# Kernel optimization log

Hardware: AMD Instinct MI355X
Metric: run time of the kernel (lower is better)

Reference implementation:

```python
import jax, jax.numpy as jnp
import numpy as np

N_ATOMS = 20000
N_CG = 1000
N_EDGES = 200000
FEAT = 128
N_RBF = 20
N_CONV = 3
CUTOFF = 5.0
EPS = 1e-15


def swish(x):
    return x * jax.nn.sigmoid(x)


def preprocess_r(r):
    # r: (n, 3) -> dist (n,), unit (n, 3)
    d = jnp.sqrt((r * r + EPS).sum(-1))
    return d, r / d[:, None]


def dist_embed(d, W, b):
    # PainnRadialBasis (learnable_k=False) + Dense + cosine envelope
    k = jnp.arange(1, N_RBF + 1, dtype=d.dtype)
    rbf = jnp.sin(k[None, :] * jnp.pi * d[:, None] / CUTOFF) / d[:, None]
    env = 0.5 * (jnp.cos(jnp.pi * d / CUTOFF) + 1.0) * (d < CUTOFF).astype(d.dtype)
    return (rbf @ W + b) * env[:, None]


def scatter_mean(x, idx, n):
    s = jax.ops.segment_sum(x, idx, num_segments=n)
    cnt = jax.ops.segment_sum(jnp.ones(idx.shape[0], x.dtype), idx, num_segments=n)
    cnt = jnp.maximum(cnt, 1.0)
    return s / cnt.reshape((n,) + (1,) * (x.ndim - 1))


def cg_encoder(z, xyz, cg_xyz, mapping, nbr_list, embed,
               msg_W1, msg_b1, msg_W2, msg_b2, msg_distW, msg_distb,
               upd_U, upd_V, upd_W1, upd_b1, upd_W2, upd_b2,
               cg_W1, cg_b1, cg_W2, cg_b2, cg_distW, cg_distb):
    s = embed[z]                                     # (N, F)
    v = jnp.zeros((s.shape[0], FEAT, 3), s.dtype)    # (N, F, 3)
    src, dst = nbr_list[:, 0], nbr_list[:, 1]
    r_ij = xyz[dst] - xyz[src]
    r_iI = xyz - cg_xyz[mapping]
    d_ij, u_ij = preprocess_r(r_ij)
    d_iI, u_iI = preprocess_r(r_iI)

    S_I = None
    V_I = None
    for i in range(N_CONV):
        # ---- MessageBlock ----
        phi = swish(s @ msg_W1[i] + msg_b1[i]) @ msg_W2[i] + msg_b2[i]          # (N, 3F)
        w_s = dist_embed(d_ij, msg_distW[i], msg_distb[i])                      # (E, 3F)
        inv = (phi[dst] * w_s).reshape(-1, 3, FEAT)                             # (E, 3, F)
        dv_ij = inv[:, 2, :, None] * u_ij[:, None, :] + inv[:, 0, :, None] * v[dst]
        s = s + jax.ops.segment_sum(inv[:, 1, :], src, num_segments=N_ATOMS)
        v = v + jax.ops.segment_sum(dv_ij, src, num_segments=N_ATOMS)
        # ---- UpdateBlock ----
        u_v = jnp.einsum('nfd,fg->ngd', v, upd_U[i])
        v_v = jnp.einsum('nfd,fg->ngd', v, upd_V[i])
        v_v_norm = jnp.sqrt((v_v * v_v + EPS).sum(-1))                          # (N, F)
        stack = swish(jnp.concatenate([s, v_v_norm], -1) @ upd_W1[i] + upd_b1[i]) @ upd_W2[i] + upd_b2[i]
        a_vv = stack[:, :FEAT, None]
        a_sv = stack[:, FEAT:2 * FEAT]
        a_ss = stack[:, 2 * FEAT:]
        v = v + u_v * a_vv
        s = s + (u_v * v_v).sum(-1) * a_sv + a_ss
        # ---- init CG features after first conv ----
        if i == 0:
            S_I = scatter_mean(s, mapping, N_CG)
            V_I = jnp.zeros((N_CG, FEAT, 3), s.dtype)
        # ---- ContractiveMessageBlock ----
        phi_cg = swish(s @ cg_W1[i] + cg_b1[i]) @ cg_W2[i] + cg_b2[i]           # (N, 3F)
        w_cg = dist_embed(d_iI, cg_distW[i], cg_distb[i])
        inv_cg = (phi_cg * w_cg).reshape(-1, 3, FEAT)
        dv_iI = inv_cg[:, 2, :, None] * u_iI[:, None, :] + inv_cg[:, 0, :, None] * v
        S_I = S_I + scatter_mean(inv_cg[:, 1, :], mapping, N_CG)
        V_I = V_I + scatter_mean(dv_iI, mapping, N_CG)
    return S_I


def setup_inputs() -> dict:
    key = jax.random.key(0)
    ks = jax.random.split(key, 20)
    p = lambda i, shape: jax.random.normal(ks[i], shape, jnp.float32) * 0.05
    return {
        'z': jax.random.randint(ks[0], (N_ATOMS,), 1, 100),
        'xyz': jax.random.normal(ks[1], (N_ATOMS, 3), jnp.float32),
        'cg_xyz': jax.random.normal(ks[2], (N_CG, 3), jnp.float32),
        'mapping': jax.random.randint(ks[3], (N_ATOMS,), 0, N_CG),
        'nbr_list': jax.random.randint(ks[4], (N_EDGES, 2), 0, N_ATOMS),
        'embed': p(5, (100, FEAT)).at[0].set(0.0),  # padding_idx=0
        'msg_W1': p(6, (N_CONV, FEAT, FEAT)), 'msg_b1': jnp.zeros((N_CONV, FEAT)),
        'msg_W2': p(7, (N_CONV, FEAT, 3 * FEAT)), 'msg_b2': jnp.zeros((N_CONV, 3 * FEAT)),
        'msg_distW': p(8, (N_CONV, N_RBF, 3 * FEAT)), 'msg_distb': jnp.zeros((N_CONV, 3 * FEAT)),
        'upd_U': p(9, (N_CONV, FEAT, FEAT)), 'upd_V': p(10, (N_CONV, FEAT, FEAT)),
        'upd_W1': p(11, (N_CONV, 2 * FEAT, FEAT)), 'upd_b1': jnp.zeros((N_CONV, FEAT)),
        'upd_W2': p(12, (N_CONV, FEAT, 3 * FEAT)), 'upd_b2': jnp.zeros((N_CONV, 3 * FEAT)),
        'cg_W1': p(13, (N_CONV, FEAT, FEAT)), 'cg_b1': jnp.zeros((N_CONV, FEAT)),
        'cg_W2': p(14, (N_CONV, FEAT, 3 * FEAT)), 'cg_b2': jnp.zeros((N_CONV, 3 * FEAT)),
        'cg_distW': p(15, (N_CONV, N_RBF, 3 * FEAT)), 'cg_distb': jnp.zeros((N_CONV, 3 * FEAT)),
    }


def reference(z, xyz, cg_xyz, mapping, nbr_list, embed,
              msg_W1, msg_b1, msg_W2, msg_b2, msg_distW, msg_distb,
              upd_U, upd_V, upd_W1, upd_b1, upd_W2, upd_b2,
              cg_W1, cg_b1, cg_W2, cg_b2, cg_distW, cg_distb):
    return cg_encoder(z, xyz, cg_xyz, mapping, nbr_list, embed,
                      msg_W1, msg_b1, msg_W2, msg_b2, msg_distW, msg_distb,
                      upd_U, upd_V, upd_W1, upd_b1, upd_W2, upd_b2,
                      cg_W1, cg_b1, cg_W2, cg_b2, cg_distW, cg_distb)
```

## Files before the change

### kernel.cpp

```cpp
#include <hip/hip_runtime.h>
#include <math.h>

#define N_ATOMS 20000
#define N_CG    1000
#define N_EDGES 200000
#define FEAT    128
#define NRBF    20
#define NCONV   3
#define CUTOFF  5.0f
#define PLANE   (N_ATOMS * FEAT)
#define PI_F    3.14159265358979323846f
#define LDH     130

#define PACK_PER_CONV 212992

typedef __attribute__((ext_vector_type(8))) short bf16x8;
typedef __attribute__((ext_vector_type(4))) float f32x4;

__device__ __forceinline__ void split2(float x, ushort& h, ushort& l)
{
    unsigned u  = __float_as_uint(x);
    unsigned hb = (u + 0x7FFFu + ((u >> 16) & 1u)) & 0xFFFF0000u;
    float    hf = __uint_as_float(hb);
    float    lf = x - hf;
    unsigned ul = __float_as_uint(lf);
    h = (ushort)(hb >> 16);
    l = (ushort)((ul + 0x7FFFu + ((ul >> 16) & 1u)) >> 16);
}

__device__ __forceinline__ float reconP(unsigned u)
{
    return __uint_as_float(u & 0xFFFF0000u) + __uint_as_float(u << 16);
}

__device__ __forceinline__ unsigned packP(float x)
{
    ushort h, l;
    split2(x, h, l);
    return ((unsigned)h << 16) | l;
}

__device__ __forceinline__ void splitv8(const float* hv, bf16x8& ah, bf16x8& al)
{
#pragma unroll
    for (int j = 0; j < 8; ++j) {
        ushort h, l;
        split2(hv[j], h, l);
        ah[j] = (short)h; al[j] = (short)l;
    }
}

__device__ __forceinline__ void unpack8(const unsigned* __restrict__ p,
                                        bf16x8& ah, bf16x8& al)
{
#pragma unroll
    for (int j = 0; j < 8; ++j) {
        unsigned u = p[j];
        ah[j] = (short)(u >> 16);
        al[j] = (short)(u & 0xFFFFu);
    }
}

#define MFMA3(ACC, AH_, AL_, BH_, BL_)                                              \
    ACC = __builtin_amdgcn_mfma_f32_16x16x32_bf16(AH_, BH_, ACC, 0, 0, 0);          \
    ACC = __builtin_amdgcn_mfma_f32_16x16x32_bf16(AH_, BL_, ACC, 0, 0, 0);          \
    ACC = __builtin_amdgcn_mfma_f32_16x16x32_bf16(AL_, BH_, ACC, 0, 0, 0);

template<int K1, int N2>
__global__ __launch_bounds__(256)
void mlp_fused(const ushort* __restrict__ AH, const ushort* __restrict__ AL,
               const ushort* __restrict__ B1h, const ushort* __restrict__ B1l,
               const float* __restrict__ b1,
               const ushort* __restrict__ B2h, const ushort* __restrict__ B2l,
               const float* __restrict__ b2, int bcol0,
               float* __restrict__ C)
{
    __shared__ float Hs[32 * LDH];
    const int tid  = threadIdx.x;
    const int lane = tid & 63;
    const int w    = tid >> 6;
    const int wm   = w & 1, wn = w >> 1;
    const int m0   = blockIdx.x * 32;
    const int l15  = lane & 15;
    const int koff = (lane >> 4) * 8;
    const int rowb = wm * 16;
    const int q4   = (lane >> 4) * 4;

    f32x4 acc1[4];
#pragma unroll
    for (int j = 0; j < 4; ++j) acc1[j] = (f32x4){0.f, 0.f, 0.f, 0.f};
    for (int k0 = 0; k0 < K1; k0 += 32) {
        size_t aa = (size_t)(m0 + rowb + l15) * K1 + k0 + koff;
        bf16x8 ah = *reinterpret_cast<const bf16x8*>(AH + aa);
        bf16x8 al = *reinterpret_cast<const bf16x8*>(AL + aa);
#pragma unroll
        for (int nf = 0; nf < 4; ++nf) {
            size_t ba = (size_t)(wn * 64 + nf * 16 + l15) * K1 + k0 + koff;
            bf16x8 bh = *reinterpret_cast<const bf16x8*>(B1h + ba);
            bf16x8 bl = *reinterpret_cast<const bf16x8*>(B1l + ba);
            MFMA3(acc1[nf], ah, al, bh, bl);
        }
    }
#pragma unroll
    for (int nf = 0; nf < 4; ++nf) {
        int col = wn * 64 + nf * 16 + l15;
        float bv = b1[col];
#pragma unroll
        for (int r = 0; r < 4; ++r) {
            float x = acc1[nf][r] + bv;
            x = x / (1.f + __expf(-x));
            Hs[(rowb + q4 + r) * LDH + col] = x;
        }
    }
    __syncthreads();

    constexpr int NF2  = N2 / 32;
    constexpr int WCOL = N2 / 2;
    f32x4 acc2[NF2];
#pragma unroll
    for (int j = 0; j < NF2; ++j) acc2[j] = (f32x4){0.f, 0.f, 0.f, 0.f};
    for (int k0 = 0; k0 < 128; k0 += 32) {
        const float* hp = &Hs[(rowb + l15) * LDH + k0 + koff];
        float hv[8];
#pragma unroll
        for (int j = 0; j < 4; ++j) hv[j] = hp[j];
#pragma unroll
        for (int j = 0; j < 4; ++j) hv[4 + j] = hp[4 + j];
        bf16x8 ah, al;
        splitv8(hv, ah, al);
#pragma unroll
        for (int nf = 0; nf < NF2; ++nf) {
            size_t ba = (size_t)(wn * WCOL + nf * 16 + l15) * 128 + k0 + koff;
            bf16x8 bh = *reinterpret_cast<const bf16x8*>(B2h + ba);
            bf16x8 bl = *reinterpret_cast<const bf16x8*>(B2l + ba);
            MFMA3(acc2[nf], ah, al, bh, bl);
        }
    }
#pragma unroll
    for (int nf = 0; nf < NF2; ++nf) {
        int col = wn * WCOL + nf * 16 + l15;
        float bv = b2 ? b2[bcol0 + col] : 0.f;
#pragma unroll
        for (int r = 0; r < 4; ++r) {
            int row = m0 + rowb + q4 + r;
            C[(size_t)row * N2 + col] = acc2[nf][r] + bv;
        }
    }
}

__global__ __launch_bounds__(256)
void k_update_mega(unsigned* __restrict__ vP,
                   const ushort* __restrict__ catH, const ushort* __restrict__ catL,
                   const ushort* __restrict__ BVh, const ushort* __restrict__ BVl,
                   const ushort* __restrict__ W1h, const ushort* __restrict__ W1l,
                   const float*  __restrict__ b1,
                   const ushort* __restrict__ W2h, const ushort* __restrict__ W2l,
                   const float*  __restrict__ b2,
                   const ushort* __restrict__ BUh, const ushort* __restrict__ BUl,
                   float* __restrict__ s,
                   ushort* __restrict__ sH, ushort* __restrict__ sL)
{
    __shared__ float  Hs[32 * LDH];
    __shared__ ushort nH[32 * 128];
    __shared__ ushort nL[32 * 128];

    const int tid  = threadIdx.x;
    const int lane = tid & 63;
    const int w    = tid >> 6;
    const int wm   = w & 1, wn = w >> 1;
    const int m0   = blockIdx.x * 32;
    const int l15  = lane & 15;
    const int koff = (lane >> 4) * 8;
    const int rowb = wm * 16;
    const int q4   = (lane >> 4) * 4;

    f32x4 accV[3][4], accU[3][4];
#pragma unroll
    for (int d = 0; d < 3; ++d)
#pragma unroll
        for (int j = 0; j < 4; ++j) {
            accV[d][j] = (f32x4){0.f, 0.f, 0.f, 0.f};
            accU[d][j] = (f32x4){0.f, 0.f, 0.f, 0.f};
        }
    for (int k0 = 0; k0 < 128; k0 += 32) {
        bf16x8 ah[3], al[3];
#pragma unroll
        for (int d = 0; d < 3; ++d) {
            size_t aa = (size_t)d * PLANE + (size_t)(m0 + rowb + l15) * 128 + k0 + koff;
            unsigned u[8];
#pragma unroll
            for (int j = 0; j < 8; ++j) u[j] = vP[aa + j];
            unpack8(u, ah[d], al[d]);
        }
#pragma unroll
        for (int nf = 0; nf < 4; ++nf) {
            size_t ba = (size_t)(wn * 64 + nf * 16 + l15) * 128 + k0 + koff;
            bf16x8 bvh = *reinterpret_cast<const bf16x8*>(BVh + ba);
            bf16x8 bvl = *reinterpret_cast<const bf16x8*>(BVl + ba);
            bf16x8 buh = *reinterpret_cast<const bf16x8*>(BUh + ba);
            bf16x8 bul = *reinterpret_cast<const bf16x8*>(BUl + ba);
#pragma unroll
            for (int d = 0; d < 3; ++d) {
                MFMA3(accV[d][nf], ah[d], al[d], bvh, bvl);
            }
#pragma unroll
            for (int d = 0; d < 3; ++d) {
                MFMA3(accU[d][nf], ah[d], al[d], buh, bul);
            }
        }
    }
#pragma unroll
    for (int nf = 0; nf < 4; ++nf) {
        int col = wn * 64 + nf * 16 + l15;
#pragma unroll
        for (int r = 0; r < 4; ++r) {
            int lrow = rowb + q4 + r;
            float x = accV[0][nf][r], y = accV[1][nf][r], z = accV[2][nf][r];
            float nrm = sqrtf(x * x + y * y + z * z + 3e-15f);
            ushort h, l;
            split2(nrm, h, l);
            nH[lrow * 128 + col] = h;
            nL[lrow * 128 + col] = l;
        }
    }
    __syncthreads();

    f32x4 acc1[4];
#pragma unroll
    for (int j = 0; j < 4; ++j) acc1[j] = (f32x4){0.f, 0.f, 0.f, 0.f};
    for (int k0 = 0; k0 < 256; k0 += 32) {
        bf16x8 ah, al;
        if (k0 < 128) {
            size_t aa = (size_t)(m0 + rowb + l15) * 128 + k0 + koff;
            ah = *reinterpret_cast<const bf16x8*>(catH + aa);
            al = *reinterpret_cast<const bf16x8*>(catL + aa);
        } else {
            int la = (rowb + l15) * 128 + (k0 - 128) + koff;
            ah = *reinterpret_cast<const bf16x8*>(nH + la);
            al = *reinterpret_cast<const bf16x8*>(nL + la);
        }
#pragma unroll
        for (int nf = 0; nf < 4; ++nf) {
            size_t ba = (size_t)(wn * 64 + nf * 16 + l15) * 256 + k0 + koff;
            bf16x8 bh = *reinterpret_cast<const bf16x8*>(W1h + ba);
            bf16x8 bl = *reinterpret_cast<const bf16x8*>(W1l + ba);
            MFMA3(acc1[nf], ah, al, bh, bl);
        }
    }
#pragma unroll
    for (int nf = 0; nf < 4; ++nf) {
        int col = wn * 64 + nf * 16 + l15;
        float bv = b1[col];
#pragma unroll
        for (int r = 0; r < 4; ++r) {
            float x = acc1[nf][r] + bv;
            x = x / (1.f + __expf(-x));
            Hs[(rowb + q4 + r) * LDH + col] = x;
        }
    }
    __syncthreads();

    f32x4 acc2[12];
#pragma unroll
    for (int j = 0; j < 12; ++j) acc2[j] = (f32x4){0.f, 0.f, 0.f, 0.f};
    for (int k0 = 0; k0 < 128; k0 += 32) {
        const float* hp = &Hs[(rowb + l15) * LDH + k0 + koff];
        float hv[8];
#pragma unroll
        for (int j = 0; j < 8; ++j) hv[j] = hp[j];
        bf16x8 ah, al;
        splitv8(hv, ah, al);
#pragma unroll
        for (int g = 0; g < 3; ++g) {
#pragma unroll
            for (int j = 0; j < 4; ++j) {
                size_t ba = (size_t)(g * 128 + wn * 64 + j * 16 + l15) * 128 + k0 + koff;
                bf16x8 bh = *reinterpret_cast<const bf16x8*>(W2h + ba);
                bf16x8 bl = *reinterpret_cast<const bf16x8*>(W2l + ba);
                MFMA3(acc2[g * 4 + j], ah, al, bh, bl);
            }
        }
    }

#pragma unroll
    for (int nf = 0; nf < 4; ++nf) {
        int col = wn * 64 + nf * 16 + l15;
        float bavv = b2[col];
        float basv = b2[128 + col];
        float bass = b2[256 + col];
#pragma unroll
        for (int r = 0; r < 4; ++r) {
            int row = m0 + rowb + q4 + r;
            size_t idx = (size_t)row * FEAT + col;
            float avv = acc2[nf][r]     + bavv;
            float asv = acc2[4 + nf][r] + basv;
            float ass = acc2[8 + nf][r] + bass;
            float u0 = accU[0][nf][r], u1 = accU[1][nf][r], u2 = accU[2][nf][r];
            float w0 = accV[0][nf][r], w1 = accV[1][nf][r], w2 = accV[2][nf][r];
            float dot = u0 * w0 + u1 * w1 + u2 * w2;
            float n0 = reconP(vP[idx])                      + u0 * avv;
            float n1 = reconP(vP[PLANE + idx])              + u1 * avv;
            float n2 = reconP(vP[2 * (size_t)PLANE + idx])  + u2 * avv;
            vP[idx] = packP(n0);
            vP[PLANE + idx] = packP(n1);
            vP[2 * (size_t)PLANE + idx] = packP(n2);
            float ns = s[idx] + dot * asv + ass;
            s[idx] = ns;
            ushort h, l;
            split2(ns, h, l); sH[idx] = h; sL[idx] = l;
        }
    }
}

__global__ void k_pack_all(const float* __restrict__ msg_W1, const float* __restrict__ msg_W2,
                           const float* __restrict__ upd_V,  const float* __restrict__ upd_W1,
                           const float* __restrict__ upd_W2, const float* __restrict__ upd_U,
                           const float* __restrict__ cg_W1,  const float* __restrict__ cg_W2,
                           ushort* __restrict__ Bh, ushort* __restrict__ Bl)
{
    const int wid = blockIdx.y, conv = blockIdx.z;
    const float* W; int K, N, ldw, col0; size_t off;
    switch (wid) {
        case 0: W = msg_W1 + (size_t)conv * 16384; K = 128; N = 128; ldw = 128; col0 = 0;   off = 0;      break;
        case 1: W = msg_W2 + (size_t)conv * 49152; K = 128; N = 384; ldw = 384; col0 = 0;   off = 16384;  break;
        case 2: W = upd_V  + (size_t)conv * 16384; K = 128; N = 128; ldw = 128; col0 = 0;   off = 65536;  break;
        case 3: W = upd_W1 + (size_t)conv * 32768; K = 256; N = 128; ldw = 128; col0 = 0;   off = 81920;  break;
        case 4: W = upd_W2 + (size_t)conv * 49152; K = 128; N = 384; ldw = 384; col0 = 0;   off = 114688; break;
        case 5: W = upd_U  + (size_t)conv * 16384; K = 128; N = 128; ldw = 128; col0 = 0;   off = 163840; break;
        case 6: W = cg_W1  + (size_t)conv * 16384; K = 128; N = 128; ldw = 128; col0 = 0;   off = 180224; break;
        default:W = cg_W2  + (size_t)conv * 49152; K = 128; N = 128; ldw = 384; col0 = 128; off = 196608; break;
    }
    off += (size_t)conv * PACK_PER_CONV;
    int idx = blockIdx.x * 256 + threadIdx.x;
    if (idx >= K * N) return;
    int k = idx & (K - 1);
    int n = idx >> ((K == 256) ? 8 : 7);
    ushort h, l;
    split2(W[(size_t)k * ldw + col0 + n], h, l);
    Bh[off + (size_t)n * K + k] = h;
    Bl[off + (size_t)n * K + k] = l;
}

__global__ void k_s_init(const int* __restrict__ z, const float* __restrict__ embed,
                         float* __restrict__ s, ushort* __restrict__ sH, ushort* __restrict__ sL)
{
    int idx = blockIdx.x * blockDim.x + threadIdx.x;
    if (idx >= PLANE) return;
    int n = idx >> 7, g = idx & 127;
    float e = embed[z[n] * FEAT + g];
    s[idx] = e;
    ushort h, l;
    split2(e, h, l);
    sH[idx] = h; sL[idx] = l;
}

__global__ void k_atom_geo(const int* __restrict__ mapping,
                           const float* __restrict__ xyz, const float* __restrict__ cg_xyz,
                           float* __restrict__ rbf_a, float* __restrict__ env_a,
                           float* __restrict__ cnt)
{
    int n = blockIdx.x * blockDim.x + threadIdx.x;
    if (n >= N_ATOMS) return;
    int m = mapping[n];
    float dx = xyz[n * 3 + 0] - cg_xyz[m * 3 + 0];
    float dy = xyz[n * 3 + 1] - cg_xyz[m * 3 + 1];
    float dz = xyz[n * 3 + 2] - cg_xyz[m * 3 + 2];
    float d = sqrtf(dx * dx + dy * dy + dz * dz + 3e-15f);
    float env = (d < CUTOFF) ? 0.5f * (cosf(PI_F * d / CUTOFF) + 1.f) : 0.f;
    env_a[n] = env;
    float s = env / d;
#pragma unroll
    for (int k = 0; k < NRBF; ++k)
        rbf_a[n * NRBF + k] = sinf((k + 1) * PI_F * d / CUTOFF) * s;
    atomicAdd(&cnt[m], 1.f);
}

__global__ void k_deg(const int* __restrict__ nbr, int* __restrict__ deg)
{
    int e = blockIdx.x * blockDim.x + threadIdx.x;
    if (e < N_EDGES) atomicAdd(&deg[nbr[2 * e]], 1);
}

__global__ __launch_bounds__(1024)
void k_scan(const int* __restrict__ deg, int* __restrict__ rowptr)
{
    __shared__ int sh[1024];
    const int chunk = (N_ATOMS + 1023) / 1024;
    int t = threadIdx.x;
    int base = t * chunk;
    int sum = 0;
    for (int i = 0; i < chunk; ++i) {
        int idx = base + i;
        if (idx < N_ATOMS) sum += deg[idx];
    }
    sh[t] = sum;
    __syncthreads();
    for (int off = 1; off < 1024; off <<= 1) {
        int val = (t >= off) ? sh[t - off] : 0;
        __syncthreads();
        sh[t] += val;
        __syncthreads();
    }
    int run = (t == 0) ? 0 : sh[t - 1];
    for (int i = 0; i < chunk; ++i) {
        int idx = base + i;
        if (idx < N_ATOMS) { rowptr[idx] = run; run += deg[idx]; }
    }
}

__global__ void k_fill(const int* __restrict__ nbr, const float* __restrict__ xyz,
                       const int* __restrict__ rowptr, int* __restrict__ cursor,
                       int* __restrict__ rec_dst, float4* __restrict__ rec_u4,
                       float* __restrict__ rec_rbf)
{
    int e = blockIdx.x * blockDim.x + threadIdx.x;
    if (e >= N_EDGES) return;
    int src = nbr[2 * e], dst = nbr[2 * e + 1];
    int pos = atomicAdd(&cursor[src], 1);
    int q = rowptr[src] + pos;
    float dx = xyz[dst * 3 + 0] - xyz[src * 3 + 0];
    float dy = xyz[dst * 3 + 1] - xyz[src * 3 + 1];
    float dz = xyz[dst * 3 + 2] - xyz[src * 3 + 2];
    float d = sqrtf(dx * dx + dy * dy + dz * dz + 3e-15f);
    float env = (d < CUTOFF) ? 0.5f * (cosf(PI_F * d / CUTOFF) + 1.f) : 0.f;
    rec_dst[q] = dst;
    rec_u4[q] = make_float4(dx / d, dy / d, dz / d, env);
    float sc = env / d;
#pragma unroll
    for (int k = 0; k < NRBF; ++k)
        rec_rbf[(size_t)q * NRBF + k] = sinf((k + 1) * PI_F * d / CUTOFF) * sc;
}

#define EDGE_BLOCKS 2500
__global__ __launch_bounds__(512, 2)
void k_edge_seg(const int* __restrict__ rowptr, const int* __restrict__ deg,
                const int* __restrict__ rec_dst, const float4* __restrict__ rec_u4,
                const float* __restrict__ rec_rbf,
                const float* __restrict__ phi,
                const unsigned* __restrict__ vPi, unsigned* __restrict__ vPo,
                float* __restrict__ s,
                ushort* __restrict__ catH, ushort* __restrict__ catL,
                const float* __restrict__ distW, const float* __restrict__ distb)
{
    const int tid    = threadIdx.x;
    const int slot   = tid >> 7;
    const int f      = tid & 127;
    const int slot_g = blockIdx.x * 4 + slot;
    const int nslots = EDGE_BLOCKS * 4;

    float wx[21], wy[21], wz[21];
#pragma unroll
    for (int k = 0; k < NRBF; ++k) {
        wx[k] = distW[k * 384 + f];
        wy[k] = distW[k * 384 + 128 + f];
        wz[k] = distW[k * 384 + 256 + f];
    }
    wx[20] = distb[f];
    wy[20] = distb[128 + f];
    wz[20] = distb[256 + f];
#pragma unroll
    for (int k = 0; k < 21; ++k) {
        asm volatile("" : "+v"(wx[k]), "+v"(wy[k]), "+v"(wz[k]));
    }

    for (int a = slot_g; a < N_ATOMS; a += nslots) {
        const int beg = rowptr[a];
        const int end = beg + deg[a];
        float s_acc = 0.f, vx = 0.f, vy = 0.f, vz = 0.f;

        for (int p = beg; p < end; p += 2) {
            const int  has2 = (p + 1 < end);
            const int  p1   = has2 ? p + 1 : p;
            const float m1  = has2 ? 1.f : 0.f;

            float4 u40 = rec_u4[p];
            float4 u41 = rec_u4[p1];
            int dst0 = rec_dst[p];
            int dst1 = rec_dst[p1];

            const float* ph0 = phi + (size_t)dst0 * 384 + f;
            const float* ph1 = phi + (size_t)dst1 * 384 + f;
            float p00 = ph0[0], p01 = ph0[128], p02 = ph0[256];
            float p10 = ph1[0], p11 = ph1[128], p12 = ph1[256];
            size_t di0 = (size_t)dst0 * FEAT + f;
            size_t di1 = (size_t)dst1 * FEAT + f;
            float v0x = reconP(vPi[di0]);
            float v0y = reconP(vPi[PLANE + di0]);
            float v0z = reconP(vPi[2 * (size_t)PLANE + di0]);
            float v1x = reconP(vPi[di1]);
            float v1y = reconP(vPi[PLANE + di1]);
            float v1z = reconP(vPi[2 * (size_t)PLANE + di1]);
            const float4* rb0 = reinterpret_cast<const float4*>(rec_rbf + (size_t)p  * NRBF);
            const float4* rb1 = reinterpret_cast<const float4*>(rec_rbf + (size_t)p1 * NRBF);
            float4 a0 = rb0[0], a1 = rb0[1], a2 = rb0[2], a3 = rb0[3], a4 = rb0[4];
            float4 b0 = rb1[0], b1 = rb1[1], b2 = rb1[2], b3 = rb1[3], b4 = rb1[4];

            const float rr0[21] = {a0.x, a0.y, a0.z, a0.w, a1.x, a1.y, a1.z, a1.w,
                                   a2.x, a2.y, a2.z, a2.w, a3.x, a3.y, a3.z, a3.w,
                                   a4.x, a4.y, a4.z, a4.w, u40.w};
            const float rr1[21] = {b0.x, b0.y, b0.z, b0.w, b1.x, b1.y, b1.z, b1.w,
                                   b2.x, b2.y, b2.z, b2.w, b3.x, b3.y, b3.z, b3.w,
                                   b4.x, b4.y, b4.z, b4.w, u41.w};
            float w00 = 0.f, w01 = 0.f, w02 = 0.f;
            float w10 = 0.f, w11 = 0.f, w12 = 0.f;
#pragma unroll
            for (int k = 0; k < 21; ++k) {
                w00 += rr0[k] * wx[k];
                w01 += rr0[k] * wy[k];
                w02 += rr0[k] * wz[k];
                w10 += rr1[k] * wx[k];
                w11 += rr1[k] * wy[k];
                w12 += rr1[k] * wz[k];
            }
            float i00 = p00 * w00, i01 = p01 * w01, i02 = p02 * w02;
            float i10 = (p10 * w10) * m1, i11 = (p11 * w11) * m1, i12 = (p12 * w12) * m1;
            vx += i02 * u40.x + i00 * v0x;
            vy += i02 * u40.y + i00 * v0y;
            vz += i02 * u40.z + i00 * v0z;
            s_acc += i01;
            vx += i12 * u41.x + i10 * v1x;
            vy += i12 * u41.y + i10 * v1y;
            vz += i12 * u41.z + i10 * v1z;
            s_acc += i11;
        }

        size_t si = (size_t)a * FEAT + f;
        float ns = s[si] + s_acc;
        s[si] = ns;
        float nx = reconP(vPi[si])                     + vx;
        float ny = reconP(vPi[PLANE + si])             + vy;
        float nz = reconP(vPi[2 * (size_t)PLANE + si]) + vz;
        vPo[si] = packP(nx);
        vPo[PLANE + si] = packP(ny);
        vPo[2 * (size_t)PLANE + si] = packP(nz);
        ushort h, l;
        split2(ns, h, l);
        catH[(size_t)a * 128 + f] = h;
        catL[(size_t)a * 128 + f] = l;
    }
}

__global__ __launch_bounds__(128)
void k_cg_msg(const int* __restrict__ mapping, const float* __restrict__ phi_mid,
              const float* __restrict__ rbf_a, const float* __restrict__ env_a,
              const float* __restrict__ distW, const float* __restrict__ distb,
              const float* __restrict__ s_add, float* __restrict__ S_acc)
{
    int n = blockIdx.x;
    float env = env_a[n];
    int f = threadIdx.x;
    if (env == 0.f && s_add == nullptr) return;
    float val = s_add ? s_add[n * FEAT + f] : 0.f;
    if (env != 0.f) {
        __shared__ float sh_rbf[NRBF];
        if (f < NRBF) sh_rbf[f] = rbf_a[n * NRBF + f];
        __syncthreads();
        float w1 = 0.f;
#pragma unroll
        for (int k = 0; k < NRBF; ++k)
            w1 += sh_rbf[k] * distW[k * 384 + 128 + f];
        w1 += distb[128 + f] * env;
        val += phi_mid[n * FEAT + f] * w1;
    }
    atomicAdd(&S_acc[mapping[n] * FEAT + f], val);
}

__global__ void k_finalize(const float* __restrict__ S_acc, const float* __restrict__ cnt,
                           float* __restrict__ out, int add)
{
    int idx = blockIdx.x * blockDim.x + threadIdx.x;
    if (idx >= N_CG * FEAT) return;
    float val = S_acc[idx] / fmaxf(cnt[idx >> 7], 1.f);
    if (add) out[idx] += val;
    else     out[idx] = val;
}

extern "C" void kernel_launch(void* const* d_in, const int* in_sizes, int n_in,
                              void* d_out, int out_size, void* d_ws, size_t ws_size,
                              hipStream_t stream)
{
    const int*   z        = (const int*)d_in[0];
    const float* xyz      = (const float*)d_in[1];
    const float* cg_xyz   = (const float*)d_in[2];
    const int*   mapping  = (const int*)d_in[3];
    const int*   nbr      = (const int*)d_in[4];
    const float* embed    = (const float*)d_in[5];
    const float* msg_W1   = (const float*)d_in[6];
    const float* msg_b1   = (const float*)d_in[7];
    const float* msg_W2   = (const float*)d_in[8];
    const float* msg_b2   = (const float*)d_in[9];
    const float* msg_dW   = (const float*)d_in[10];
    const float* msg_db   = (const float*)d_in[11];
    const float* upd_U    = (const float*)d_in[12];
    const float* upd_V    = (const float*)d_in[13];
    const float* upd_W1   = (const float*)d_in[14];
    const float* upd_b1   = (const float*)d_in[15];
    const float* upd_W2   = (const float*)d_in[16];
    const float* upd_b2   = (const float*)d_in[17];
    const float* cg_W1    = (const float*)d_in[18];
    const float* cg_b1    = (const float*)d_in[19];
    const float* cg_W2    = (const float*)d_in[20];
    const float* cg_b2    = (const float*)d_in[21];
    const float* cg_dW    = (const float*)d_in[22];
    const float* cg_db    = (const float*)d_in[23];
    float* out = (float*)d_out;

    float* ws = (float*)d_ws;
    size_t o = 0;
    float* s      = ws + o; o += PLANE;
    float* uv     = ws + o; o += PLANE;
    float* phi    = ws + o; o += (size_t)N_ATOMS * 384;
    float* catpk  = ws + o; o += PLANE;
    float* spk    = ws + o; o += PLANE;
    unsigned* vPA = (unsigned*)(ws + o); o += 3 * PLANE;
    unsigned* vPB = (unsigned*)(ws + o); o += 3 * PLANE;
    float4* rec_u4 = (float4*)(ws + o); o += (size_t)N_EDGES * 4;
    float* rec_rbf = ws + o; o += (size_t)N_EDGES * NRBF;
    int*   rec_dst = (int*)(ws + o); o += N_EDGES;
    float* rbf_a  = ws + o; o += (size_t)N_ATOMS * NRBF;
    float* env_a  = ws + o; o += N_ATOMS;
    float* cnt    = ws + o; o += N_CG;
    float* S_acc  = ws + o; o += N_CG * FEAT;
    int*   deg    = (int*)(ws + o); o += N_ATOMS;
    int*   rowptr = (int*)(ws + o); o += N_ATOMS;
    int*   cursor = (int*)(ws + o); o += N_ATOMS;
    ushort* packH = (ushort*)(ws + o); o += (size_t)NCONV * PACK_PER_CONV / 2;
    ushort* packL = (ushort*)(ws + o); o += (size_t)NCONV * PACK_PER_CONV / 2;

    ushort* catH = (ushort*)catpk; ushort* catL = catH + (size_t)N_ATOMS * 128;
    ushort* sH = (ushort*)spk;  ushort* sL = sH + PLANE;

    hipMemsetAsync(vPA, 0, sizeof(unsigned) * 3 * PLANE, stream);
    hipMemsetAsync(cnt, 0, sizeof(float) * N_CG, stream);
    hipMemsetAsync(deg, 0, sizeof(int) * N_ATOMS, stream);
    hipMemsetAsync(cursor, 0, sizeof(int) * N_ATOMS, stream);
    k_pack_all<<<dim3(192, 8, 3), 256, 0, stream>>>(msg_W1, msg_W2, upd_V, upd_W1,
                                                    upd_W2, upd_U, cg_W1, cg_W2,
                                                    packH, packL);
    k_s_init<<<(PLANE + 255) / 256, 256, 0, stream>>>(z, embed, s, sH, sL);
    k_atom_geo<<<(N_ATOMS + 255) / 256, 256, 0, stream>>>(mapping, xyz, cg_xyz,
                                                          rbf_a, env_a, cnt);
    k_deg<<<(N_EDGES + 255) / 256, 256, 0, stream>>>(nbr, deg);
    k_scan<<<1, 1024, 0, stream>>>(deg, rowptr);
    k_fill<<<(N_EDGES + 255) / 256, 256, 0, stream>>>(nbr, xyz, rowptr, cursor,
                                                      rec_dst, rec_u4, rec_rbf);

    unsigned* vPc = vPA;
    unsigned* vPn = vPB;

    for (int i = 0; i < NCONV; ++i) {
        const float* mb1 = msg_b1 + (size_t)i * FEAT;
        const float* mb2 = msg_b2 + (size_t)i * 384;
        const float* mdW = msg_dW + (size_t)i * NRBF * 384;
        const float* mdb = msg_db + (size_t)i * 384;
        const float* ub1 = upd_b1 + (size_t)i * FEAT;
        const float* ub2 = upd_b2 + (size_t)i * 384;
        const float* cb1 = cg_b1  + (size_t)i * FEAT;
        const float* cb2 = cg_b2  + (size_t)i * 384;
        const float* cdW = cg_dW  + (size_t)i * NRBF * 384;
        const float* cdb = cg_db  + (size_t)i * 384;
        const size_t pb  = (size_t)i * PACK_PER_CONV;

        mlp_fused<128, 384><<<625, 256, 0, stream>>>(
            sH, sL, packH + pb + 0, packL + pb + 0, mb1,
            packH + pb + 16384, packL + pb + 16384, mb2, 0, phi);
        k_edge_seg<<<EDGE_BLOCKS, 512, 0, stream>>>(rowptr, deg, rec_dst, rec_u4,
                                                    rec_rbf, phi, vPc, vPn, s,
                                                    catH, catL, mdW, mdb);

        k_update_mega<<<625, 256, 0, stream>>>(
            vPn, catH, catL,
            packH + pb + 65536,  packL + pb + 65536,
            packH + pb + 81920,  packL + pb + 81920,
            ub1,
            packH + pb + 114688, packL + pb + 114688,
            ub2,
            packH + pb + 163840, packL + pb + 163840,
            s, sH, sL);

        mlp_fused<128, 128><<<625, 256, 0, stream>>>(
            sH, sL, packH + pb + 180224, packL + pb + 180224, cb1,
            packH + pb + 196608, packL + pb + 196608, cb2, 128, uv);
        hipMemsetAsync(S_acc, 0, sizeof(float) * N_CG * FEAT, stream);
        k_cg_msg<<<N_ATOMS, 128, 0, stream>>>(mapping, uv, rbf_a, env_a, cdW, cdb,
                                              (i == 0) ? s : nullptr, S_acc);
        k_finalize<<<(N_CG * FEAT + 255) / 256, 256, 0, stream>>>(S_acc, cnt, out,
                                                                  i == 0 ? 0 : 1);

        unsigned* t = vPn; vPn = vPc; vPc = t;
    }
}
```

Measured before the change: 1.384 ms.

## Fuse next-layer message MLP with CG MLP into one dual kernel

```diff
diff --git a/kernel.cpp b/kernel.cpp
--- a/kernel.cpp
+++ b/kernel.cpp
@@ -89,6 +89,7 @@
     f32x4 acc1[4];
 #pragma unroll
     for (int j = 0; j < 4; ++j) acc1[j] = (f32x4){0.f, 0.f, 0.f, 0.f};
+#pragma unroll
     for (int k0 = 0; k0 < K1; k0 += 32) {
         size_t aa = (size_t)(m0 + rowb + l15) * K1 + k0 + koff;
         bf16x8 ah = *reinterpret_cast<const bf16x8*>(AH + aa);
@@ -119,13 +120,12 @@
     f32x4 acc2[NF2];
 #pragma unroll
     for (int j = 0; j < NF2; ++j) acc2[j] = (f32x4){0.f, 0.f, 0.f, 0.f};
+#pragma unroll
     for (int k0 = 0; k0 < 128; k0 += 32) {
         const float* hp = &Hs[(rowb + l15) * LDH + k0 + koff];
         float hv[8];
 #pragma unroll
-        for (int j = 0; j < 4; ++j) hv[j] = hp[j];
-#pragma unroll
-        for (int j = 0; j < 4; ++j) hv[4 + j] = hp[4 + j];
+        for (int j = 0; j < 8; ++j) hv[j] = hp[j];
         bf16x8 ah, al;
         splitv8(hv, ah, al);
 #pragma unroll
@@ -144,6 +144,120 @@
         for (int r = 0; r < 4; ++r) {
             int row = m0 + rowb + q4 + r;
             C[(size_t)row * N2 + col] = acc2[nf][r] + bv;
+        }
+    }
+}
+
+__global__ __launch_bounds__(256)
+void mlp_dual(const ushort* __restrict__ AH, const ushort* __restrict__ AL,
+              const ushort* __restrict__ B1mh, const ushort* __restrict__ B1ml,
+              const float* __restrict__ b1m,
+              const ushort* __restrict__ B2mh, const ushort* __restrict__ B2ml,
+              const float* __restrict__ b2m,
+              const ushort* __restrict__ B1ch, const ushort* __restrict__ B1cl,
+              const float* __restrict__ b1c,
+              const ushort* __restrict__ B2ch, const ushort* __restrict__ B2cl,
+              const float* __restrict__ b2c,
+              float* __restrict__ Cm, float* __restrict__ Cc)
+{
+    __shared__ float Hm[32 * LDH];
+    __shared__ float Hc[32 * LDH];
+    const int tid  = threadIdx.x;
+    const int lane = tid & 63;
+    const int w    = tid >> 6;
+    const int wm   = w & 1, wn = w >> 1;
+    const int m0   = blockIdx.x * 32;
+    const int l15  = lane & 15;
+    const int koff = (lane >> 4) * 8;
+    const int rowb = wm * 16;
+    const int q4   = (lane >> 4) * 4;
+
+    f32x4 am[4], ac[4];
+#pragma unroll
+    for (int j = 0; j < 4; ++j) {
+        am[j] = (f32x4){0.f, 0.f, 0.f, 0.f};
+        ac[j] = (f32x4){0.f, 0.f, 0.f, 0.f};
+    }
+#pragma unroll
+    for (int k0 = 0; k0 < 128; k0 += 32) {
+        size_t aa = (size_t)(m0 + rowb + l15) * 128 + k0 + koff;
+        bf16x8 ah = *reinterpret_cast<const bf16x8*>(AH + aa);
+        bf16x8 al = *reinterpret_cast<const bf16x8*>(AL + aa);
+#pragma unroll
+        for (int nf = 0; nf < 4; ++nf) {
+            size_t ba = (size_t)(wn * 64 + nf * 16 + l15) * 128 + k0 + koff;
+            bf16x8 bmh = *reinterpret_cast<const bf16x8*>(B1mh + ba);
+            bf16x8 bml = *reinterpret_cast<const bf16x8*>(B1ml + ba);
+            MFMA3(am[nf], ah, al, bmh, bml);
+            bf16x8 bch = *reinterpret_cast<const bf16x8*>(B1ch + ba);
+            bf16x8 bcl = *reinterpret_cast<const bf16x8*>(B1cl + ba);
+            MFMA3(ac[nf], ah, al, bch, bcl);
+        }
+    }
+#pragma unroll
+    for (int nf = 0; nf < 4; ++nf) {
+        int col = wn * 64 + nf * 16 + l15;
+        float bvm = b1m[col];
+        float bvc = b1c[col];
+#pragma unroll
+        for (int r = 0; r < 4; ++r) {
+            int lr = rowb + q4 + r;
+            float x = am[nf][r] + bvm;
+            Hm[lr * LDH + col] = x / (1.f + __expf(-x));
+            float y = ac[nf][r] + bvc;
+            Hc[lr * LDH + col] = y / (1.f + __expf(-y));
+        }
+    }
+    __syncthreads();
+
+    f32x4 a2m[12], a2c[4];
+#pragma unroll
+    for (int j = 0; j < 12; ++j) a2m[j] = (f32x4){0.f, 0.f, 0.f, 0.f};
+#pragma unroll
+    for (int j = 0; j < 4; ++j)  a2c[j] = (f32x4){0.f, 0.f, 0.f, 0.f};
+#pragma unroll
+    for (int k0 = 0; k0 < 128; k0 += 32) {
+        const float* hpm = &Hm[(rowb + l15) * LDH + k0 + koff];
+        const float* hpc = &Hc[(rowb + l15) * LDH + k0 + koff];
+        float hvm[8], hvc[8];
+#pragma unroll
+        for (int j = 0; j < 8; ++j) { hvm[j] = hpm[j]; hvc[j] = hpc[j]; }
+        bf16x8 ahm, alm, ahc, alc;
+        splitv8(hvm, ahm, alm);
+        splitv8(hvc, ahc, alc);
+#pragma unroll
+        for (int nf = 0; nf < 12; ++nf) {
+            size_t ba = (size_t)(wn * 192 + nf * 16 + l15) * 128 + k0 + koff;
+            bf16x8 bh = *reinterpret_cast<const bf16x8*>(B2mh + ba);
+            bf16x8 bl = *reinterpret_cast<const bf16x8*>(B2ml + ba);
+            MFMA3(a2m[nf], ahm, alm, bh, bl);
+        }
+#pragma unroll
+        for (int nf = 0; nf < 4; ++nf) {
+            size_t ba = (size_t)(wn * 64 + nf * 16 + l15) * 128 + k0 + koff;
+            bf16x8 bh = *reinterpret_cast<const bf16x8*>(B2ch + ba);
+            bf16x8 bl = *reinterpret_cast<const bf16x8*>(B2cl + ba);
+            MFMA3(a2c[nf], ahc, alc, bh, bl);
+        }
+    }
+#pragma unroll
+    for (int nf = 0; nf < 12; ++nf) {
+        int col = wn * 192 + nf * 16 + l15;
+        float bv = b2m[col];
+#pragma unroll
+        for (int r = 0; r < 4; ++r) {
+            int row = m0 + rowb + q4 + r;
+            Cm[(size_t)row * 384 + col] = a2m[nf][r] + bv;
+        }
+    }
+#pragma unroll
+    for (int nf = 0; nf < 4; ++nf) {
+        int col = wn * 64 + nf * 16 + l15;
+        float bv = b2c[128 + col];
+#pragma unroll
+        for (int r = 0; r < 4; ++r) {
+            int row = m0 + rowb + q4 + r;
+            Cc[(size_t)row * 128 + col] = a2c[nf][r] + bv;
         }
     }
 }
@@ -228,6 +342,7 @@
     f32x4 acc1[4];
 #pragma unroll
     for (int j = 0; j < 4; ++j) acc1[j] = (f32x4){0.f, 0.f, 0.f, 0.f};
+#pragma unroll 2
     for (int k0 = 0; k0 < 256; k0 += 32) {
         bf16x8 ah, al;
         if (k0 < 128) {
@@ -648,22 +763,21 @@
     unsigned* vPc = vPA;
     unsigned* vPn = vPB;
 
+    mlp_fused<128, 384><<<625, 256, 0, stream>>>(
+        sH, sL, packH + 0, packL + 0, msg_b1,
+        packH + 16384, packL + 16384, msg_b2, 0, phi);
+
     for (int i = 0; i < NCONV; ++i) {
-        const float* mb1 = msg_b1 + (size_t)i * FEAT;
-        const float* mb2 = msg_b2 + (size_t)i * 384;
+        const float* ub1 = upd_b1 + (size_t)i * FEAT;
+        const float* ub2 = upd_b2 + (size_t)i * 384;
         const float* mdW = msg_dW + (size_t)i * NRBF * 384;
         const float* mdb = msg_db + (size_t)i * 384;
-        const float* ub1 = upd_b1 + (size_t)i * FEAT;
-        const float* ub2 = upd_b2 + (size_t)i * 384;
         const float* cb1 = cg_b1  + (size_t)i * FEAT;
         const float* cb2 = cg_b2  + (size_t)i * 384;
         const float* cdW = cg_dW  + (size_t)i * NRBF * 384;
         const float* cdb = cg_db  + (size_t)i * 384;
         const size_t pb  = (size_t)i * PACK_PER_CONV;
 
-        mlp_fused<128, 384><<<625, 256, 0, stream>>>(
-            sH, sL, packH + pb + 0, packL + pb + 0, mb1,
-            packH + pb + 16384, packL + pb + 16384, mb2, 0, phi);
         k_edge_seg<<<EDGE_BLOCKS, 512, 0, stream>>>(rowptr, deg, rec_dst, rec_u4,
                                                     rec_rbf, phi, vPc, vPn, s,
                                                     catH, catL, mdW, mdb);
@@ -678,9 +792,21 @@
             packH + pb + 163840, packL + pb + 163840,
             s, sH, sL);
 
-        mlp_fused<128, 128><<<625, 256, 0, stream>>>(
-            sH, sL, packH + pb + 180224, packL + pb + 180224, cb1,
-            packH + pb + 196608, packL + pb + 196608, cb2, 128, uv);
+        if (i < NCONV - 1) {
+            const size_t pn = (size_t)(i + 1) * PACK_PER_CONV;
+            mlp_dual<<<625, 256, 0, stream>>>(
+                sH, sL,
+                packH + pn + 0,      packL + pn + 0,      msg_b1 + (size_t)(i + 1) * FEAT,
+                packH + pn + 16384,  packL + pn + 16384,  msg_b2 + (size_t)(i + 1) * 384,
+                packH + pb + 180224, packL + pb + 180224, cb1,
+                packH + pb + 196608, packL + pb + 196608, cb2,
+                phi, uv);
+        } else {
+            mlp_fused<128, 128><<<625, 256, 0, stream>>>(
+                sH, sL, packH + pb + 180224, packL + pb + 180224, cb1,
+                packH + pb + 196608, packL + pb + 196608, cb2, 128, uv);
+        }
+
         hipMemsetAsync(S_acc, 0, sizeof(float) * N_CG * FEAT, stream);
         k_cg_msg<<<N_ATOMS, 128, 0, stream>>>(mapping, uv, rbf_a, env_a, cdW, cdb,
                                               (i == 0) ? s : nullptr, S_acc);
```

New measurement: 1.301 ms. 1.06x faster.
